# Kernel optimization log

Measured on AMD Instinct MI355X. Metric: run time of the kernel, lower is better.

The kernel has to match this reference:

```python
import jax, jax.numpy as jnp
import numpy as np

E = 8          # num_experts
K = 2          # num_experts_per_tok
NORM_TOPK = True
B, S, D, F = 2, 1024, 2048, 1024  # batch, seq, hidden, moe_intermediate


def _kaiming_uniform(key, shape):
    # moe_fused_kaiming_uniform_: bound = sqrt(3*5 / in_features), in_features = shape[-1]
    bound = float(np.sqrt(3.0 * 5.0 / shape[-1]))
    return jax.random.uniform(key, shape, jnp.float32, -bound, bound)


def setup_inputs() -> dict:
    key = jax.random.key(0)
    k0, k1, k2, k3, k4 = jax.random.split(key, 5)
    gate_bound = float(1.0 / np.sqrt(D))  # nn.Linear default init
    return {
        "hidden_states": jax.random.normal(k0, (B, S, D), jnp.float32),
        "gate_w": jax.random.uniform(k1, (E, D), jnp.float32, -gate_bound, gate_bound),
        "w_gate_proj": _kaiming_uniform(k2, (E, F, D)),
        "w_up_proj": _kaiming_uniform(k3, (E, F, D)),
        "w_down_proj": _kaiming_uniform(k4, (E, D, F)),
    }


def reference(hidden_states, gate_w, w_gate_proj, w_up_proj, w_down_proj):
    b, s, d = hidden_states.shape
    x = hidden_states.reshape(-1, d)                      # [T, D]
    T = x.shape[0]

    # Router: softmax in fp32, top-k, optional renorm
    router_logits = x @ gate_w.T                          # [T, E]
    probs = jax.nn.softmax(router_logits.astype(jnp.float32), axis=-1)
    routing_weights, selected = jax.lax.top_k(probs, K)   # [T, K], [T, K]
    if NORM_TOPK:
        routing_weights = routing_weights / routing_weights.sum(-1, keepdims=True)
    routing_weights = routing_weights.astype(x.dtype)

    # Dense combine weights: c[t, e] = sum_k rw[t,k] * (sel[t,k]==e)
    combine = jnp.zeros((T, E), x.dtype).at[jnp.arange(T)[:, None], selected].add(routing_weights)

    # Expert SwiGLU FFN (dense over experts; combine zeros out unrouted experts,
    # identical math to sorted grouped-GEMM dispatch in the original)
    g = jnp.einsum('td,efd->tef', x, w_gate_proj)         # [T, E, F]
    u = jnp.einsum('td,efd->tef', x, w_up_proj)           # [T, E, F]
    h = jax.nn.silu(g) * u                                # [T, E, F]
    out = jnp.einsum('tef,edf,te->td', h, w_down_proj, combine)  # [T, D]

    return out.reshape(b, s, d), router_logits
```

## Files before the change

### kernel.cpp

```cpp
#include <hip/hip_runtime.h>
#include <stdint.h>

#define T_TOK 2048
#define DIM   2048
#define FDIM  1024
#define NE    8
#define MAXTILES 40

typedef __attribute__((ext_vector_type(8))) short short8;
typedef __attribute__((ext_vector_type(4))) float f32x4;

__device__ __forceinline__ unsigned short f2b(float f) {
  union { float f; unsigned int i; } x; x.f = f;
  unsigned int r = x.i + 0x7fffu + ((x.i >> 16) & 1u);
  return (unsigned short)(r >> 16);
}

__device__ __forceinline__ void async16(void* lds, const void* g) {
  __builtin_amdgcn_global_load_lds(
      (const __attribute__((address_space(1))) void*)g,
      (__attribute__((address_space(3))) void*)lds, 16, 0, 0);
}

__global__ __launch_bounds__(256) void cvt_w_k(const float* __restrict__ src,
                                               unsigned short* __restrict__ dst)
{
  size_t i = ((size_t)blockIdx.x * 256 + threadIdx.x) * 8;
  float4 a = *(const float4*)(src + i);
  float4 b = *(const float4*)(src + i + 4);
  ushort4 o0, o1;
  o0.x = f2b(a.x); o0.y = f2b(a.y); o0.z = f2b(a.z); o0.w = f2b(a.w);
  o1.x = f2b(b.x); o1.y = f2b(b.y); o1.z = f2b(b.z); o1.w = f2b(b.w);
  *(ushort4*)(dst + i) = o0;
  *(ushort4*)(dst + i + 4) = o1;
}

__global__ __launch_bounds__(256) void router_k(
    const float* __restrict__ x, const float* __restrict__ gw,
    float* __restrict__ topkw, int* __restrict__ topke, int* __restrict__ counts,
    float* __restrict__ logits_out, unsigned short* __restrict__ xb)
{
  int wave = threadIdx.x >> 6, lane = threadIdx.x & 63;
  int t = blockIdx.x * 4 + wave;
  const float* xr = x + (size_t)t * DIM;
  unsigned short* xbr = xb + (size_t)t * DIM;
  float acc[NE];
#pragma unroll
  for (int e = 0; e < NE; e++) acc[e] = 0.f;
  for (int d = lane * 4; d < DIM; d += 256) {
    float4 xv = *(const float4*)(xr + d);
    ushort4 xo;
    xo.x = f2b(xv.x); xo.y = f2b(xv.y); xo.z = f2b(xv.z); xo.w = f2b(xv.w);
    *(ushort4*)(xbr + d) = xo;
#pragma unroll
    for (int e = 0; e < NE; e++) {
      float4 gv = *(const float4*)(gw + e * DIM + d);
      acc[e] += xv.x * gv.x + xv.y * gv.y + xv.z * gv.z + xv.w * gv.w;
    }
  }
#pragma unroll
  for (int off = 32; off > 0; off >>= 1) {
#pragma unroll
    for (int e = 0; e < NE; e++) acc[e] += __shfl_down(acc[e], off);
  }
  if (lane == 0) {
    float m = acc[0];
#pragma unroll
    for (int e = 1; e < NE; e++) m = fmaxf(m, acc[e]);
    float p[NE];
#pragma unroll
    for (int e = 0; e < NE; e++) p[e] = __expf(acc[e] - m);
    int e0 = 0;
#pragma unroll
    for (int e = 1; e < NE; e++) if (acc[e] > acc[e0]) e0 = e;
    int e1 = -1;
#pragma unroll
    for (int e = 0; e < NE; e++) if (e != e0 && (e1 < 0 || acc[e] > acc[e1])) e1 = e;
    float s = p[e0] + p[e1];
    topkw[t * 2] = p[e0] / s;
    topkw[t * 2 + 1] = p[e1] / s;
    topke[t * 2] = e0; topke[t * 2 + 1] = e1;
    atomicAdd(&counts[e0], 1);
    atomicAdd(&counts[e1], 1);
#pragma unroll
    for (int e = 0; e < NE; e++) logits_out[t * NE + e] = acc[e];
  }
}

__global__ void scan_k(const int* __restrict__ counts, int* __restrict__ offsets,
                       int* __restrict__ cursors, int4* __restrict__ tiles,
                       int* __restrict__ ntiles)
{
  if (threadIdx.x == 0 && blockIdx.x == 0) {
    int o = 0, nt = 0;
    for (int e = 0; e < NE; e++) {
      offsets[e] = o; cursors[e] = o;
      int c = counts[e];
      for (int r = 0; r < c; r += 128) {
        int rows = c - r < 128 ? c - r : 128;
        tiles[nt] = make_int4(e, o + r, rows, 0);
        nt++;
      }
      o += c;
    }
    offsets[NE] = o;
    *ntiles = nt;
  }
}

__global__ void scatter_k(const int* __restrict__ topke, int* __restrict__ cursors,
                          int* __restrict__ perm)
{
  int i = blockIdx.x * blockDim.x + threadIdx.x;
  int e = topke[i];
  int s = atomicAdd(&cursors[e], 1);
  perm[s] = i;
}


__global__ __launch_bounds__(256) void gemm1_bf_k(
    const unsigned short* __restrict__ xb,
    const unsigned short* __restrict__ wgb,
    const unsigned short* __restrict__ wub,
    const int* __restrict__ perm, const float* __restrict__ topkw,
    const int4* __restrict__ tiles, const int* __restrict__ ntiles,
    unsigned short* __restrict__ H)
{
  __shared__ short As[2][128 * 32];
  __shared__ short Bgs[2][64 * 32];
  __shared__ short Bus[2][64 * 32];
  __shared__ int rowtok[128];
  __shared__ float roww[128];

  if (blockIdx.x >= *ntiles) return;
  int4 tm = tiles[blockIdx.x];
  int e = tm.x, row0 = tm.y, nrows = tm.z;
  int tid = threadIdx.x;
  if (tid < 128) {
    int r = tid < nrows ? tid : (nrows - 1);
    int pid = perm[row0 + r];
    rowtok[tid] = pid >> 1;
    roww[tid] = topkw[pid];
  }
  __syncthreads();

  int f0 = blockIdx.y * 64;
  int crow = tid >> 2;
  int ccol = (tid & 3) * 8;
  const unsigned short* a0 = xb + (size_t)rowtok[crow] * DIM + ccol;
  const unsigned short* a1 = xb + (size_t)rowtok[crow + 64] * DIM + ccol;
  const unsigned short* bg = wgb + ((size_t)e * FDIM + f0 + crow) * DIM + ccol;
  const unsigned short* bu = wub + ((size_t)e * FDIM + f0 + crow) * DIM + ccol;

  int wave = tid >> 6, lane = tid & 63;
  int wm = wave >> 1, wn = wave & 1;
  int lrow = lane & 15, quad = lane >> 4;

  f32x4 accg[4][2], accu[4][2];
#pragma unroll
  for (int i = 0; i < 4; i++)
#pragma unroll
    for (int j = 0; j < 2; j++) {
      accg[i][j] = (f32x4){0.f, 0.f, 0.f, 0.f};
      accu[i][j] = (f32x4){0.f, 0.f, 0.f, 0.f};
    }

  const int aoff = (wm * 64 + lrow) * 32 + quad * 8;
  const int boff = (wn * 32 + lrow) * 32 + quad * 8;

#define STAGE1(b, k)                                 \
  do {                                               \
    async16(&As[b][tid * 8], a0 + (k));              \
    async16(&As[b][(256 + tid) * 8], a1 + (k));      \
    async16(&Bgs[b][tid * 8], bg + (k));             \
    async16(&Bus[b][tid * 8], bu + (k));             \
  } while (0)

  STAGE1(0, 0);

#pragma unroll 1
  for (int k0 = 0; k0 < DIM; k0 += 32) {
    int b = (k0 >> 5) & 1;
    __syncthreads();
    if (k0 + 32 < DIM) STAGE1(b ^ 1, k0 + 32);
    const short* arp = &As[0][0] + b * (128 * 32) + aoff;
    const short* bgp = &Bgs[0][0] + b * (64 * 32) + boff;
    const short* bup = &Bus[0][0] + b * (64 * 32) + boff;
    short8 af[4], bgf[2], buf2[2];
#pragma unroll
    for (int i = 0; i < 4; i++) af[i] = *(const short8*)(arp + i * 16 * 32);
#pragma unroll
    for (int j = 0; j < 2; j++) {
      bgf[j]  = *(const short8*)(bgp + j * 16 * 32);
      buf2[j] = *(const short8*)(bup + j * 16 * 32);
    }
#pragma unroll
    for (int i = 0; i < 4; i++)
#pragma unroll
      for (int j = 0; j < 2; j++) {
        accg[i][j] = __builtin_amdgcn_mfma_f32_16x16x32_bf16(af[i], bgf[j], accg[i][j], 0, 0, 0);
        accu[i][j] = __builtin_amdgcn_mfma_f32_16x16x32_bf16(af[i], buf2[j], accu[i][j], 0, 0, 0);
      }
  }
#undef STAGE1

#pragma unroll
  for (int i = 0; i < 4; i++) {
#pragma unroll
    for (int reg = 0; reg < 4; reg++) {
      int r = wm * 64 + i * 16 + quad * 4 + reg;
      if (r < nrows) {
        float w = roww[r];
#pragma unroll
        for (int j = 0; j < 2; j++) {
          float g = accg[i][j][reg], u = accu[i][j][reg];
          float h = g * u * w / (1.f + __expf(-g));
          H[(size_t)(row0 + r) * FDIM + f0 + wn * 32 + j * 16 + lrow] = f2b(h);
        }
      }
    }
  }
}

__global__ __launch_bounds__(256) void gemm2_bf_k(
    const unsigned short* __restrict__ H,
    const unsigned short* __restrict__ wdb,
    const int* __restrict__ perm,
    const int4* __restrict__ tiles, const int* __restrict__ ntiles,
    float* __restrict__ out)
{
  __shared__ short Hs[2][128 * 32];
  __shared__ short Bs[2][128 * 32];
  __shared__ int rowtok[128];

  if (blockIdx.x >= *ntiles) return;
  int4 tm = tiles[blockIdx.x];
  int e = tm.x, row0 = tm.y, nrows = tm.z;
  int tid = threadIdx.x;
  if (tid < 128) {
    int r = tid < nrows ? tid : (nrows - 1);
    rowtok[tid] = perm[row0 + r] >> 1;
  }
  __syncthreads();

  int d0 = blockIdx.y * 128;
  int crow = tid >> 2, ccol = (tid & 3) * 8;
  const unsigned short* a0 = H + (size_t)(row0 + crow) * FDIM + ccol;
  const unsigned short* a1 = H + (size_t)(row0 + crow + 64) * FDIM + ccol;
  const unsigned short* b0 = wdb + ((size_t)e * DIM + d0 + crow) * FDIM + ccol;
  const unsigned short* b1 = b0 + (size_t)64 * FDIM;

  int wave = tid >> 6, lane = tid & 63;
  int wm = wave >> 1, wn = wave & 1;
  int lrow = lane & 15, quad = lane >> 4;

  f32x4 acc[4][4];
#pragma unroll
  for (int i = 0; i < 4; i++)
#pragma unroll
    for (int j = 0; j < 4; j++) acc[i][j] = (f32x4){0.f, 0.f, 0.f, 0.f};

  const int aoff = (wm * 64 + lrow) * 32 + quad * 8;
  const int boff = (wn * 64 + lrow) * 32 + quad * 8;

#define STAGE2(b, k)                                 \
  do {                                               \
    async16(&Hs[b][tid * 8], a0 + (k));              \
    async16(&Hs[b][(256 + tid) * 8], a1 + (k));      \
    async16(&Bs[b][tid * 8], b0 + (k));              \
    async16(&Bs[b][(256 + tid) * 8], b1 + (k));      \
  } while (0)

  STAGE2(0, 0);

#pragma unroll 1
  for (int k0 = 0; k0 < FDIM; k0 += 32) {
    int b = (k0 >> 5) & 1;
    __syncthreads();
    if (k0 + 32 < FDIM) STAGE2(b ^ 1, k0 + 32);
    const short* arp = &Hs[0][0] + b * (128 * 32) + aoff;
    const short* brp = &Bs[0][0] + b * (128 * 32) + boff;
    short8 af[4], bf[4];
#pragma unroll
    for (int i = 0; i < 4; i++) af[i] = *(const short8*)(arp + i * 16 * 32);
#pragma unroll
    for (int j = 0; j < 4; j++) bf[j] = *(const short8*)(brp + j * 16 * 32);
#pragma unroll
    for (int i = 0; i < 4; i++)
#pragma unroll
      for (int j = 0; j < 4; j++)
        acc[i][j] = __builtin_amdgcn_mfma_f32_16x16x32_bf16(af[i], bf[j], acc[i][j], 0, 0, 0);
  }
#undef STAGE2

#pragma unroll
  for (int i = 0; i < 4; i++) {
#pragma unroll
    for (int reg = 0; reg < 4; reg++) {
      int r = wm * 64 + i * 16 + quad * 4 + reg;
      if (r < nrows) {
        int t = rowtok[r];
#pragma unroll
        for (int j = 0; j < 4; j++) {
          atomicAdd(&out[(size_t)t * DIM + d0 + wn * 64 + j * 16 + lrow], acc[i][j][reg]);
        }
      }
    }
  }
}


__global__ __launch_bounds__(256) void gemm1_f32_k(
    const unsigned short* __restrict__ xb,
    const float* __restrict__ wg,
    const float* __restrict__ wu,
    const int* __restrict__ perm, const float* __restrict__ topkw,
    const int4* __restrict__ tiles, const int* __restrict__ ntiles,
    unsigned short* __restrict__ H)
{
  __shared__ short As[128 * 32];
  __shared__ short Bgs[64 * 32];
  __shared__ short Bus[64 * 32];
  __shared__ int rowtok[128];
  __shared__ float roww[128];

  if (blockIdx.x >= *ntiles) return;
  int4 tm = tiles[blockIdx.x];
  int e = tm.x, row0 = tm.y, nrows = tm.z;
  int tid = threadIdx.x;
  if (tid < 128) {
    int r = tid < nrows ? tid : (nrows - 1);
    int pid = perm[row0 + r];
    rowtok[tid] = pid >> 1;
    roww[tid] = topkw[pid];
  }
  __syncthreads();

  int f0 = blockIdx.y * 64;
  int crow = tid >> 2;
  int ccol = (tid & 3) * 8;
  const unsigned short* a0 = xb + (size_t)rowtok[crow] * DIM + ccol;
  const unsigned short* a1 = xb + (size_t)rowtok[crow + 64] * DIM + ccol;
  const float* bg32 = wg + ((size_t)e * FDIM + f0 + crow) * DIM + ccol;
  const float* bu32 = wu + ((size_t)e * FDIM + f0 + crow) * DIM + ccol;
  short* as0 = As + tid * 8;
  short* as1 = As + (256 + tid) * 8;

  int wave = tid >> 6, lane = tid & 63;
  int wm = wave >> 1, wn = wave & 1;
  int lrow = lane & 15, quad = lane >> 4;

  f32x4 accg[4][2], accu[4][2];
#pragma unroll
  for (int i = 0; i < 4; i++)
#pragma unroll
    for (int j = 0; j < 2; j++) {
      accg[i][j] = (f32x4){0.f, 0.f, 0.f, 0.f};
      accu[i][j] = (f32x4){0.f, 0.f, 0.f, 0.f};
    }

  const short* arp = As + (wm * 64 + lrow) * 32 + quad * 8;
  const short* bgp = Bgs + (wn * 32 + lrow) * 32 + quad * 8;
  const short* bup = Bus + (wn * 32 + lrow) * 32 + quad * 8;

#pragma unroll 1
  for (int k0 = 0; k0 < DIM; k0 += 32) {
    async16(as0, a0 + k0);
    async16(as1, a1 + k0);
    float4 g0 = *(const float4*)(bg32 + k0);
    float4 g1 = *(const float4*)(bg32 + k0 + 4);
    float4 u0 = *(const float4*)(bu32 + k0);
    float4 u1 = *(const float4*)(bu32 + k0 + 4);
    short8 gs, us;
    gs[0] = f2b(g0.x); gs[1] = f2b(g0.y); gs[2] = f2b(g0.z); gs[3] = f2b(g0.w);
    gs[4] = f2b(g1.x); gs[5] = f2b(g1.y); gs[6] = f2b(g1.z); gs[7] = f2b(g1.w);
    us[0] = f2b(u0.x); us[1] = f2b(u0.y); us[2] = f2b(u0.z); us[3] = f2b(u0.w);
    us[4] = f2b(u1.x); us[5] = f2b(u1.y); us[6] = f2b(u1.z); us[7] = f2b(u1.w);
    *(short8*)(Bgs + tid * 8) = gs;
    *(short8*)(Bus + tid * 8) = us;
    __syncthreads();
    short8 af[4], bgf[2], buf2[2];
#pragma unroll
    for (int i = 0; i < 4; i++) af[i] = *(const short8*)(arp + i * 16 * 32);
#pragma unroll
    for (int j = 0; j < 2; j++) {
      bgf[j]  = *(const short8*)(bgp + j * 16 * 32);
      buf2[j] = *(const short8*)(bup + j * 16 * 32);
    }
#pragma unroll
    for (int i = 0; i < 4; i++)
#pragma unroll
      for (int j = 0; j < 2; j++) {
        accg[i][j] = __builtin_amdgcn_mfma_f32_16x16x32_bf16(af[i], bgf[j], accg[i][j], 0, 0, 0);
        accu[i][j] = __builtin_amdgcn_mfma_f32_16x16x32_bf16(af[i], buf2[j], accu[i][j], 0, 0, 0);
      }
    __syncthreads();
  }

#pragma unroll
  for (int i = 0; i < 4; i++) {
#pragma unroll
    for (int reg = 0; reg < 4; reg++) {
      int r = wm * 64 + i * 16 + quad * 4 + reg;
      if (r < nrows) {
        float w = roww[r];
#pragma unroll
        for (int j = 0; j < 2; j++) {
          float g = accg[i][j][reg], u = accu[i][j][reg];
          float h = g * u * w / (1.f + __expf(-g));
          H[(size_t)(row0 + r) * FDIM + f0 + wn * 32 + j * 16 + lrow] = f2b(h);
        }
      }
    }
  }
}

__global__ __launch_bounds__(256) void gemm2_f32_k(
    const unsigned short* __restrict__ H,
    const float* __restrict__ wd,
    const int* __restrict__ perm,
    const int4* __restrict__ tiles, const int* __restrict__ ntiles,
    float* __restrict__ out)
{
  __shared__ short Hs[128 * 32];
  __shared__ short Bs[64 * 32];
  __shared__ int rowtok[128];

  if (blockIdx.x >= *ntiles) return;
  int4 tm = tiles[blockIdx.x];
  int e = tm.x, row0 = tm.y, nrows = tm.z;
  int tid = threadIdx.x;
  if (tid < 128) {
    int r = tid < nrows ? tid : (nrows - 1);
    rowtok[tid] = perm[row0 + r] >> 1;
  }
  __syncthreads();

  int d0 = blockIdx.y * 64;
  int crow = tid >> 2, ccol = (tid & 3) * 8;
  const unsigned short* a0 = H + (size_t)(row0 + crow) * FDIM + ccol;
  const unsigned short* a1 = H + (size_t)(row0 + crow + 64) * FDIM + ccol;
  const float* b32 = wd + ((size_t)e * DIM + d0 + crow) * FDIM + ccol;
  short* hs0 = Hs + tid * 8;
  short* hs1 = Hs + (256 + tid) * 8;

  int wave = tid >> 6, lane = tid & 63;
  int wm = wave >> 1, wn = wave & 1;
  int lrow = lane & 15, quad = lane >> 4;

  f32x4 acc[4][2];
#pragma unroll
  for (int i = 0; i < 4; i++)
#pragma unroll
    for (int j = 0; j < 2; j++) acc[i][j] = (f32x4){0.f, 0.f, 0.f, 0.f};

  const short* arp = Hs + (wm * 64 + lrow) * 32 + quad * 8;
  const short* brp = Bs + (wn * 32 + lrow) * 32 + quad * 8;

#pragma unroll 1
  for (int k0 = 0; k0 < FDIM; k0 += 32) {
    async16(hs0, a0 + k0);
    async16(hs1, a1 + k0);
    float4 b0 = *(const float4*)(b32 + k0);
    float4 b1 = *(const float4*)(b32 + k0 + 4);
    short8 bsv;
    bsv[0] = f2b(b0.x); bsv[1] = f2b(b0.y); bsv[2] = f2b(b0.z); bsv[3] = f2b(b0.w);
    bsv[4] = f2b(b1.x); bsv[5] = f2b(b1.y); bsv[6] = f2b(b1.z); bsv[7] = f2b(b1.w);
    *(short8*)(Bs + tid * 8) = bsv;
    __syncthreads();
    short8 af[4], bf[2];
#pragma unroll
    for (int i = 0; i < 4; i++) af[i] = *(const short8*)(arp + i * 16 * 32);
#pragma unroll
    for (int j = 0; j < 2; j++) bf[j] = *(const short8*)(brp + j * 16 * 32);
#pragma unroll
    for (int i = 0; i < 4; i++)
#pragma unroll
      for (int j = 0; j < 2; j++)
        acc[i][j] = __builtin_amdgcn_mfma_f32_16x16x32_bf16(af[i], bf[j], acc[i][j], 0, 0, 0);
    __syncthreads();
  }

#pragma unroll
  for (int i = 0; i < 4; i++) {
#pragma unroll
    for (int reg = 0; reg < 4; reg++) {
      int r = wm * 64 + i * 16 + quad * 4 + reg;
      if (r < nrows) {
        int t = rowtok[r];
#pragma unroll
        for (int j = 0; j < 2; j++) {
          atomicAdd(&out[(size_t)t * DIM + d0 + wn * 32 + j * 16 + lrow], acc[i][j][reg]);
        }
      }
    }
  }
}

extern "C" void kernel_launch(void* const* d_in, const int* in_sizes, int n_in,
                              void* d_out, int out_size, void* d_ws, size_t ws_size,
                              hipStream_t stream)
{
  const float* x  = (const float*)d_in[0];
  const float* gw = (const float*)d_in[1];
  const float* wg = (const float*)d_in[2];
  const float* wu = (const float*)d_in[3];
  const float* wd = (const float*)d_in[4];
  float* out = (float*)d_out;
  float* logits_out = out + (size_t)T_TOK * DIM;

  char* ws = (char*)d_ws;
  float* topkw   = (float*)(ws + 0);
  int*   topke   = (int*)(ws + 16384);
  int*   counts  = (int*)(ws + 32768);
  int*   offsets = (int*)(ws + 32768 + 64);
  int*   cursors = (int*)(ws + 32768 + 128);
  int*   ntiles  = (int*)(ws + 32768 + 192);
  int4*  tiles   = (int4*)(ws + 32768 + 256);
  int*   perm    = (int*)(ws + 32768 + 2048);
  unsigned short* xb  = (unsigned short*)(ws + (1u << 16));
  unsigned short* H   = (unsigned short*)(ws + (9u  << 20));
  unsigned short* wgb = (unsigned short*)(ws + (18u << 20));
  unsigned short* wub = (unsigned short*)(ws + (50u << 20));
  unsigned short* wdb = wgb;
  const size_t WS_NEED = (size_t)82u << 20;

  hipMemsetAsync(d_out, 0, (size_t)out_size * sizeof(float), stream);
  hipMemsetAsync(counts, 0, 64, stream);

  router_k<<<T_TOK / 4, 256, 0, stream>>>(x, gw, topkw, topke, counts, logits_out, xb);
  scan_k<<<1, 64, 0, stream>>>(counts, offsets, cursors, tiles, ntiles);
  scatter_k<<<(T_TOK * 2) / 256, 256, 0, stream>>>(topke, cursors, perm);

  if (ws_size >= WS_NEED) {
    const int nblk = (NE * FDIM * DIM) / 2048;
    cvt_w_k<<<nblk, 256, 0, stream>>>(wg, wgb);
    cvt_w_k<<<nblk, 256, 0, stream>>>(wu, wub);
    gemm1_bf_k<<<dim3(MAXTILES, FDIM / 64), 256, 0, stream>>>(xb, wgb, wub, perm, topkw, tiles, ntiles, H);
    cvt_w_k<<<nblk, 256, 0, stream>>>(wd, wdb);
    gemm2_bf_k<<<dim3(MAXTILES, DIM / 128), 256, 0, stream>>>(H, wdb, perm, tiles, ntiles, out);
  } else {
    gemm1_f32_k<<<dim3(MAXTILES, FDIM / 64), 256, 0, stream>>>(xb, wg, wu, perm, topkw, tiles, ntiles, H);
    gemm2_f32_k<<<dim3(MAXTILES, DIM / 64), 256, 0, stream>>>(H, wd, perm, tiles, ntiles, out);
  }
}
```

Before: 407.6 us.

## Use 64-row expert tiles, fuse scan/scatter, replace atomics with combine pass

Shrinks the row tile of both bf16 grouped GEMMs from 128 to 64 rows, which gives more blocks and less padding waste per expert. gemm2 now writes per-slot results to a workspace buffer O instead of doing float atomicAdds into the output. A new combine kernel then sums each token's two expert rows, which also removes the full output memset. The scan and scatter kernels are merged into a single block, and the gate and up weight conversions are merged into one launch. The cost is less B-tile reuse per block, an extra 16MB fp32 intermediate written and read back, and one more kernel launch.

```diff
diff --git a/kernel.cpp b/kernel.cpp
--- a/kernel.cpp
+++ b/kernel.cpp
@@ -5,7 +5,8 @@
 #define DIM   2048
 #define FDIM  1024
 #define NE    8
-#define MAXTILES 40
+#define MAXT64  72
+#define MAXT128 40
 
 typedef __attribute__((ext_vector_type(8))) short short8;
 typedef __attribute__((ext_vector_type(4))) float f32x4;
@@ -35,6 +36,25 @@
   *(ushort4*)(dst + i + 4) = o1;
 }
 
+__global__ __launch_bounds__(256) void cvt2_k(const float* __restrict__ sA,
+                                              unsigned short* __restrict__ dA,
+                                              const float* __restrict__ sB,
+                                              unsigned short* __restrict__ dB)
+{
+  int bid = blockIdx.x;
+  const float* src; unsigned short* dst;
+  if (bid < 8192) { src = sA; dst = dA; }
+  else            { src = sB; dst = dB; bid -= 8192; }
+  size_t i = ((size_t)bid * 256 + threadIdx.x) * 8;
+  float4 a = *(const float4*)(src + i);
+  float4 b = *(const float4*)(src + i + 4);
+  ushort4 o0, o1;
+  o0.x = f2b(a.x); o0.y = f2b(a.y); o0.z = f2b(a.z); o0.w = f2b(a.w);
+  o1.x = f2b(b.x); o1.y = f2b(b.y); o1.z = f2b(b.z); o1.w = f2b(b.w);
+  *(ushort4*)(dst + i) = o0;
+  *(ushort4*)(dst + i + 4) = o1;
+}
+
 __global__ __launch_bounds__(256) void router_k(
     const float* __restrict__ x, const float* __restrict__ gw,
     float* __restrict__ topkw, int* __restrict__ topke, int* __restrict__ counts,
@@ -87,34 +107,38 @@
   }
 }
 
-__global__ void scan_k(const int* __restrict__ counts, int* __restrict__ offsets,
-                       int* __restrict__ cursors, int4* __restrict__ tiles,
-                       int* __restrict__ ntiles)
-{
-  if (threadIdx.x == 0 && blockIdx.x == 0) {
-    int o = 0, nt = 0;
+__global__ __launch_bounds__(256) void scan_scatter_k(
+    const int* __restrict__ counts, const int* __restrict__ topke,
+    int4* __restrict__ tiles64, int* __restrict__ ntiles64,
+    int4* __restrict__ tiles128, int* __restrict__ ntiles128,
+    int* __restrict__ perm, int* __restrict__ slot_of)
+{
+  __shared__ int cur[NE];
+  int tid = threadIdx.x;
+  if (tid == 0) {
+    int o = 0, nt = 0, nt2 = 0;
     for (int e = 0; e < NE; e++) {
-      offsets[e] = o; cursors[e] = o;
+      cur[e] = o;
       int c = counts[e];
+      for (int r = 0; r < c; r += 64) {
+        int rows = c - r < 64 ? c - r : 64;
+        tiles64[nt++] = make_int4(e, o + r, rows, 0);
+      }
       for (int r = 0; r < c; r += 128) {
         int rows = c - r < 128 ? c - r : 128;
-        tiles[nt] = make_int4(e, o + r, rows, 0);
-        nt++;
+        tiles128[nt2++] = make_int4(e, o + r, rows, 0);
       }
       o += c;
     }
-    offsets[NE] = o;
-    *ntiles = nt;
-  }
-}
-
-__global__ void scatter_k(const int* __restrict__ topke, int* __restrict__ cursors,
-                          int* __restrict__ perm)
-{
-  int i = blockIdx.x * blockDim.x + threadIdx.x;
-  int e = topke[i];
-  int s = atomicAdd(&cursors[e], 1);
-  perm[s] = i;
+    *ntiles64 = nt; *ntiles128 = nt2;
+  }
+  __syncthreads();
+  for (int i = tid; i < T_TOK * 2; i += 256) {
+    int e = topke[i];
+    int s = atomicAdd(&cur[e], 1);
+    perm[s] = i;
+    slot_of[i] = s;
+  }
 }
 
 
@@ -126,17 +150,17 @@
     const int4* __restrict__ tiles, const int* __restrict__ ntiles,
     unsigned short* __restrict__ H)
 {
-  __shared__ short As[2][128 * 32];
+  __shared__ short As[2][64 * 32];
   __shared__ short Bgs[2][64 * 32];
   __shared__ short Bus[2][64 * 32];
-  __shared__ int rowtok[128];
-  __shared__ float roww[128];
+  __shared__ int rowtok[64];
+  __shared__ float roww[64];
 
   if (blockIdx.x >= *ntiles) return;
   int4 tm = tiles[blockIdx.x];
   int e = tm.x, row0 = tm.y, nrows = tm.z;
   int tid = threadIdx.x;
-  if (tid < 128) {
+  if (tid < 64) {
     int r = tid < nrows ? tid : (nrows - 1);
     int pid = perm[row0 + r];
     rowtok[tid] = pid >> 1;
@@ -148,7 +172,6 @@
   int crow = tid >> 2;
   int ccol = (tid & 3) * 8;
   const unsigned short* a0 = xb + (size_t)rowtok[crow] * DIM + ccol;
-  const unsigned short* a1 = xb + (size_t)rowtok[crow + 64] * DIM + ccol;
   const unsigned short* bg = wgb + ((size_t)e * FDIM + f0 + crow) * DIM + ccol;
   const unsigned short* bu = wub + ((size_t)e * FDIM + f0 + crow) * DIM + ccol;
 
@@ -156,22 +179,21 @@
   int wm = wave >> 1, wn = wave & 1;
   int lrow = lane & 15, quad = lane >> 4;
 
-  f32x4 accg[4][2], accu[4][2];
-#pragma unroll
-  for (int i = 0; i < 4; i++)
+  f32x4 accg[2][2], accu[2][2];
+#pragma unroll
+  for (int i = 0; i < 2; i++)
 #pragma unroll
     for (int j = 0; j < 2; j++) {
       accg[i][j] = (f32x4){0.f, 0.f, 0.f, 0.f};
       accu[i][j] = (f32x4){0.f, 0.f, 0.f, 0.f};
     }
 
-  const int aoff = (wm * 64 + lrow) * 32 + quad * 8;
+  const int aoff = (wm * 32 + lrow) * 32 + quad * 8;
   const int boff = (wn * 32 + lrow) * 32 + quad * 8;
 
 #define STAGE1(b, k)                                 \
   do {                                               \
     async16(&As[b][tid * 8], a0 + (k));              \
-    async16(&As[b][(256 + tid) * 8], a1 + (k));      \
     async16(&Bgs[b][tid * 8], bg + (k));             \
     async16(&Bus[b][tid * 8], bu + (k));             \
   } while (0)
@@ -183,19 +205,19 @@
     int b = (k0 >> 5) & 1;
     __syncthreads();
     if (k0 + 32 < DIM) STAGE1(b ^ 1, k0 + 32);
-    const short* arp = &As[0][0] + b * (128 * 32) + aoff;
+    const short* arp = &As[0][0]  + b * (64 * 32) + aoff;
     const short* bgp = &Bgs[0][0] + b * (64 * 32) + boff;
     const short* bup = &Bus[0][0] + b * (64 * 32) + boff;
-    short8 af[4], bgf[2], buf2[2];
-#pragma unroll
-    for (int i = 0; i < 4; i++) af[i] = *(const short8*)(arp + i * 16 * 32);
+    short8 af[2], bgf[2], buf2[2];
+#pragma unroll
+    for (int i = 0; i < 2; i++) af[i] = *(const short8*)(arp + i * 16 * 32);
 #pragma unroll
     for (int j = 0; j < 2; j++) {
       bgf[j]  = *(const short8*)(bgp + j * 16 * 32);
       buf2[j] = *(const short8*)(bup + j * 16 * 32);
     }
 #pragma unroll
-    for (int i = 0; i < 4; i++)
+    for (int i = 0; i < 2; i++)
 #pragma unroll
       for (int j = 0; j < 2; j++) {
         accg[i][j] = __builtin_amdgcn_mfma_f32_16x16x32_bf16(af[i], bgf[j], accg[i][j], 0, 0, 0);
@@ -205,10 +227,10 @@
 #undef STAGE1
 
 #pragma unroll
-  for (int i = 0; i < 4; i++) {
+  for (int i = 0; i < 2; i++) {
 #pragma unroll
     for (int reg = 0; reg < 4; reg++) {
-      int r = wm * 64 + i * 16 + quad * 4 + reg;
+      int r = wm * 32 + i * 16 + quad * 4 + reg;
       if (r < nrows) {
         float w = roww[r];
 #pragma unroll
@@ -225,28 +247,20 @@
 __global__ __launch_bounds__(256) void gemm2_bf_k(
     const unsigned short* __restrict__ H,
     const unsigned short* __restrict__ wdb,
-    const int* __restrict__ perm,
     const int4* __restrict__ tiles, const int* __restrict__ ntiles,
-    float* __restrict__ out)
-{
-  __shared__ short Hs[2][128 * 32];
+    float* __restrict__ O)
+{
+  __shared__ short Hs[2][64 * 32];
   __shared__ short Bs[2][128 * 32];
-  __shared__ int rowtok[128];
 
   if (blockIdx.x >= *ntiles) return;
   int4 tm = tiles[blockIdx.x];
   int e = tm.x, row0 = tm.y, nrows = tm.z;
   int tid = threadIdx.x;
-  if (tid < 128) {
-    int r = tid < nrows ? tid : (nrows - 1);
-    rowtok[tid] = perm[row0 + r] >> 1;
-  }
-  __syncthreads();
 
   int d0 = blockIdx.y * 128;
   int crow = tid >> 2, ccol = (tid & 3) * 8;
   const unsigned short* a0 = H + (size_t)(row0 + crow) * FDIM + ccol;
-  const unsigned short* a1 = H + (size_t)(row0 + crow + 64) * FDIM + ccol;
   const unsigned short* b0 = wdb + ((size_t)e * DIM + d0 + crow) * FDIM + ccol;
   const unsigned short* b1 = b0 + (size_t)64 * FDIM;
 
@@ -254,19 +268,18 @@
   int wm = wave >> 1, wn = wave & 1;
   int lrow = lane & 15, quad = lane >> 4;
 
-  f32x4 acc[4][4];
-#pragma unroll
-  for (int i = 0; i < 4; i++)
+  f32x4 acc[2][4];
+#pragma unroll
+  for (int i = 0; i < 2; i++)
 #pragma unroll
     for (int j = 0; j < 4; j++) acc[i][j] = (f32x4){0.f, 0.f, 0.f, 0.f};
 
-  const int aoff = (wm * 64 + lrow) * 32 + quad * 8;
+  const int aoff = (wm * 32 + lrow) * 32 + quad * 8;
   const int boff = (wn * 64 + lrow) * 32 + quad * 8;
 
 #define STAGE2(b, k)                                 \
   do {                                               \
     async16(&Hs[b][tid * 8], a0 + (k));              \
-    async16(&Hs[b][(256 + tid) * 8], a1 + (k));      \
     async16(&Bs[b][tid * 8], b0 + (k));              \
     async16(&Bs[b][(256 + tid) * 8], b1 + (k));      \
   } while (0)
@@ -278,15 +291,15 @@
     int b = (k0 >> 5) & 1;
     __syncthreads();
     if (k0 + 32 < FDIM) STAGE2(b ^ 1, k0 + 32);
-    const short* arp = &Hs[0][0] + b * (128 * 32) + aoff;
+    const short* arp = &Hs[0][0] + b * (64 * 32) + aoff;
     const short* brp = &Bs[0][0] + b * (128 * 32) + boff;
-    short8 af[4], bf[4];
-#pragma unroll
-    for (int i = 0; i < 4; i++) af[i] = *(const short8*)(arp + i * 16 * 32);
+    short8 af[2], bf[4];
+#pragma unroll
+    for (int i = 0; i < 2; i++) af[i] = *(const short8*)(arp + i * 16 * 32);
 #pragma unroll
     for (int j = 0; j < 4; j++) bf[j] = *(const short8*)(brp + j * 16 * 32);
 #pragma unroll
-    for (int i = 0; i < 4; i++)
+    for (int i = 0; i < 2; i++)
 #pragma unroll
       for (int j = 0; j < 4; j++)
         acc[i][j] = __builtin_amdgcn_mfma_f32_16x16x32_bf16(af[i], bf[j], acc[i][j], 0, 0, 0);
@@ -294,19 +307,35 @@
 #undef STAGE2
 
 #pragma unroll
-  for (int i = 0; i < 4; i++) {
+  for (int i = 0; i < 2; i++) {
 #pragma unroll
     for (int reg = 0; reg < 4; reg++) {
-      int r = wm * 64 + i * 16 + quad * 4 + reg;
+      int r = wm * 32 + i * 16 + quad * 4 + reg;
       if (r < nrows) {
-        int t = rowtok[r];
 #pragma unroll
         for (int j = 0; j < 4; j++) {
-          atomicAdd(&out[(size_t)t * DIM + d0 + wn * 64 + j * 16 + lrow], acc[i][j][reg]);
+          O[(size_t)(row0 + r) * DIM + d0 + wn * 64 + j * 16 + lrow] = acc[i][j][reg];
         }
       }
     }
   }
+}
+
+__global__ __launch_bounds__(256) void combine_k(
+    const float* __restrict__ O, const int* __restrict__ slot_of,
+    float* __restrict__ out)
+{
+  int t = blockIdx.x;
+  int d = threadIdx.x * 8;
+  int s0 = slot_of[2 * t], s1 = slot_of[2 * t + 1];
+  const float4* p0 = (const float4*)(O + (size_t)s0 * DIM + d);
+  const float4* p1 = (const float4*)(O + (size_t)s1 * DIM + d);
+  float4 a0 = p0[0], a1 = p0[1], c0 = p1[0], c1 = p1[1];
+  float4 r0, r1;
+  r0.x = a0.x + c0.x; r0.y = a0.y + c0.y; r0.z = a0.z + c0.z; r0.w = a0.w + c0.w;
+  r1.x = a1.x + c1.x; r1.y = a1.y + c1.y; r1.z = a1.z + c1.z; r1.w = a1.w + c1.w;
+  float4* po = (float4*)(out + (size_t)t * DIM + d);
+  po[0] = r0; po[1] = r1;
 }
 
 
@@ -510,37 +539,38 @@
   float* logits_out = out + (size_t)T_TOK * DIM;
 
   char* ws = (char*)d_ws;
-  float* topkw   = (float*)(ws + 0);
-  int*   topke   = (int*)(ws + 16384);
-  int*   counts  = (int*)(ws + 32768);
-  int*   offsets = (int*)(ws + 32768 + 64);
-  int*   cursors = (int*)(ws + 32768 + 128);
-  int*   ntiles  = (int*)(ws + 32768 + 192);
-  int4*  tiles   = (int4*)(ws + 32768 + 256);
-  int*   perm    = (int*)(ws + 32768 + 2048);
-  unsigned short* xb  = (unsigned short*)(ws + (1u << 16));
+  float* topkw    = (float*)(ws + 0);
+  int*   topke    = (int*)(ws + 16384);
+  int*   counts   = (int*)(ws + 32768);
+  int*   ntiles64 = (int*)(ws + 32832);
+  int*   ntiles128= (int*)(ws + 32836);
+  int4*  tiles64  = (int4*)(ws + 33024);
+  int4*  tiles128 = (int4*)(ws + 34304);
+  int*   perm     = (int*)(ws + 35072);
+  int*   slot_of  = (int*)(ws + 51456);
+  unsigned short* xb  = (unsigned short*)(ws + 131072);
   unsigned short* H   = (unsigned short*)(ws + (9u  << 20));
   unsigned short* wgb = (unsigned short*)(ws + (18u << 20));
   unsigned short* wub = (unsigned short*)(ws + (50u << 20));
   unsigned short* wdb = wgb;
+  float* O = (float*)(ws + (50u << 20));
   const size_t WS_NEED = (size_t)82u << 20;
 
-  hipMemsetAsync(d_out, 0, (size_t)out_size * sizeof(float), stream);
   hipMemsetAsync(counts, 0, 64, stream);
 
   router_k<<<T_TOK / 4, 256, 0, stream>>>(x, gw, topkw, topke, counts, logits_out, xb);
-  scan_k<<<1, 64, 0, stream>>>(counts, offsets, cursors, tiles, ntiles);
-  scatter_k<<<(T_TOK * 2) / 256, 256, 0, stream>>>(topke, cursors, perm);
+  scan_scatter_k<<<1, 256, 0, stream>>>(counts, topke, tiles64, ntiles64,
+                                        tiles128, ntiles128, perm, slot_of);
 
   if (ws_size >= WS_NEED) {
-    const int nblk = (NE * FDIM * DIM) / 2048;
-    cvt_w_k<<<nblk, 256, 0, stream>>>(wg, wgb);
-    cvt_w_k<<<nblk, 256, 0, stream>>>(wu, wub);
-    gemm1_bf_k<<<dim3(MAXTILES, FDIM / 64), 256, 0, stream>>>(xb, wgb, wub, perm, topkw, tiles, ntiles, H);
-    cvt_w_k<<<nblk, 256, 0, stream>>>(wd, wdb);
-    gemm2_bf_k<<<dim3(MAXTILES, DIM / 128), 256, 0, stream>>>(H, wdb, perm, tiles, ntiles, out);
+    cvt2_k<<<16384, 256, 0, stream>>>(wg, wgb, wu, wub);
+    gemm1_bf_k<<<dim3(MAXT64, FDIM / 64), 256, 0, stream>>>(xb, wgb, wub, perm, topkw, tiles64, ntiles64, H);
+    cvt_w_k<<<8192, 256, 0, stream>>>(wd, wdb);
+    gemm2_bf_k<<<dim3(MAXT64, DIM / 128), 256, 0, stream>>>(H, wdb, tiles64, ntiles64, O);
+    combine_k<<<T_TOK, 256, 0, stream>>>(O, slot_of, out);
   } else {
-    gemm1_f32_k<<<dim3(MAXTILES, FDIM / 64), 256, 0, stream>>>(xb, wg, wu, perm, topkw, tiles, ntiles, H);
-    gemm2_f32_k<<<dim3(MAXTILES, DIM / 64), 256, 0, stream>>>(H, wd, perm, tiles, ntiles, out);
-  }
-}
+    hipMemsetAsync(d_out, 0, (size_t)T_TOK * DIM * sizeof(float), stream);
+    gemm1_f32_k<<<dim3(MAXT128, FDIM / 64), 256, 0, stream>>>(xb, wg, wu, perm, topkw, tiles128, ntiles128, H);
+    gemm2_f32_k<<<dim3(MAXT128, DIM / 64), 256, 0, stream>>>(H, wd, perm, tiles128, ntiles128, out);
+  }
+}
```

Measured after the change: 444.0 us. 8.9% more time.
